# Kernel optimization log

Hardware: AMD Instinct MI355X
Metric: run time of the kernel (lower is better)

Reference implementation:

```python
import jax, jax.numpy as jnp
import numpy as np

W = 4096          # n_wavelengths
S = 4096          # n_spatial_modes
N_KEYS = 1024     # number of stored memories
SHARPNESS = 10.0  # config.retrieval_sharpness


def setup_inputs() -> dict:
    key = jax.random.key(0)
    k = jax.random.split(key, 6)
    return {
        "holo_re": jax.random.normal(k[0], (W, S), dtype=jnp.float32),
        "holo_im": jax.random.normal(k[1], (W, S), dtype=jnp.float32),
        "cue_re": jax.random.normal(k[2], (W, S), dtype=jnp.float32),
        "cue_im": jax.random.normal(k[3], (W, S), dtype=jnp.float32),
        "keys_re": jax.random.normal(k[4], (N_KEYS, W), dtype=jnp.float32),
        "keys_im": jax.random.normal(k[5], (N_KEYS, W), dtype=jnp.float32),
    }


def reference(holo_re, holo_im, cue_re, cue_im, keys_re, keys_im):
    hologram = holo_re + 1j * holo_im      # [W, S] complex64
    cue = cue_re + 1j * cue_im             # [W, S]
    keys = keys_re + 1j * keys_im          # [N, W]
    # noisy_mix = (hologram * cue.conj()).sum(dim=1)
    noisy_mix = jnp.sum(hologram * jnp.conj(cue), axis=1)  # [W]
    # torch.dot does NOT conjugate: plain complex dot per key -> batched matvec
    correlations = jnp.abs(keys @ noisy_mix)               # [N]
    attention = jax.nn.softmax(correlations * SHARPNESS)   # [N] real
    clean_key = attention.astype(keys.dtype) @ keys        # [W] complex
    out = hologram * clean_key[:, None]                    # [W, S] complex
    # return real/imag stacked so the harness compares real arrays
    return jnp.stack([out.real, out.imag])                 # [2, W, S] float32
```

## Files before the change

### kernel.cpp

```cpp
#include <hip/hip_runtime.h>
#include <math.h>

#define WDIM 4096
#define SDIM 4096
#define NKEYS 1024
#define SHARP 10.0f

__device__ __forceinline__ float wave_reduce_sum(float v) {
#pragma unroll
    for (int off = 32; off > 0; off >>= 1) v += __shfl_down(v, off, 64);
    return v;
}

__global__ __launch_bounds__(256) void k_mix(
    const float* __restrict__ hr, const float* __restrict__ hi,
    const float* __restrict__ cr, const float* __restrict__ ci,
    float* __restrict__ mix_re, float* __restrict__ mix_im) {
    const int w = blockIdx.x;
    const size_t base = (size_t)w * SDIM;
    const float4* hr4 = (const float4*)(hr + base);
    const float4* hi4 = (const float4*)(hi + base);
    const float4* cr4 = (const float4*)(cr + base);
    const float4* ci4 = (const float4*)(ci + base);
    float sr = 0.f, si = 0.f;
#pragma unroll
    for (int i = threadIdx.x; i < SDIM / 4; i += 256) {
        float4 a = hr4[i], b = hi4[i], c = cr4[i], d = ci4[i];
        sr += a.x * c.x + b.x * d.x;  si += b.x * c.x - a.x * d.x;
        sr += a.y * c.y + b.y * d.y;  si += b.y * c.y - a.y * d.y;
        sr += a.z * c.z + b.z * d.z;  si += b.z * c.z - a.z * d.z;
        sr += a.w * c.w + b.w * d.w;  si += b.w * c.w - a.w * d.w;
    }
    sr = wave_reduce_sum(sr);
    si = wave_reduce_sum(si);
    __shared__ float lre[4], lim[4];
    const int wave = threadIdx.x >> 6, lane = threadIdx.x & 63;
    if (lane == 0) { lre[wave] = sr; lim[wave] = si; }
    __syncthreads();
    if (threadIdx.x == 0) {
        mix_re[w] = lre[0] + lre[1] + lre[2] + lre[3];
        mix_im[w] = lim[0] + lim[1] + lim[2] + lim[3];
    }
}

__global__ __launch_bounds__(256) void k_corr(
    const float* __restrict__ kr, const float* __restrict__ ki,
    const float* __restrict__ mr, const float* __restrict__ mi,
    float* __restrict__ corr) {
    const int n = blockIdx.x;
    const size_t base = (size_t)n * WDIM;
    const float4* kr4 = (const float4*)(kr + base);
    const float4* ki4 = (const float4*)(ki + base);
    const float4* mr4 = (const float4*)mr;
    const float4* mi4 = (const float4*)mi;
    float zr = 0.f, zi = 0.f;
#pragma unroll
    for (int i = threadIdx.x; i < WDIM / 4; i += 256) {
        float4 a = kr4[i], b = ki4[i], m = mr4[i], q = mi4[i];
        zr += a.x * m.x - b.x * q.x;  zi += a.x * q.x + b.x * m.x;
        zr += a.y * m.y - b.y * q.y;  zi += a.y * q.y + b.y * m.y;
        zr += a.z * m.z - b.z * q.z;  zi += a.z * q.z + b.z * m.z;
        zr += a.w * m.w - b.w * q.w;  zi += a.w * q.w + b.w * m.w;
    }
    zr = wave_reduce_sum(zr);
    zi = wave_reduce_sum(zi);
    __shared__ float lre[4], lim[4];
    const int wave = threadIdx.x >> 6, lane = threadIdx.x & 63;
    if (lane == 0) { lre[wave] = zr; lim[wave] = zi; }
    __syncthreads();
    if (threadIdx.x == 0) {
        const float fr = lre[0] + lre[1] + lre[2] + lre[3];
        const float fi = lim[0] + lim[1] + lim[2] + lim[3];
        corr[n] = sqrtf(fr * fr + fi * fi) * SHARP;
    }
}

__global__ __launch_bounds__(256) void k_softmax(
    const float* __restrict__ corr, float* __restrict__ att) {
    const int t = threadIdx.x;
    __shared__ float red[256];
    float v[4];
    float m = -1e30f;
#pragma unroll
    for (int j = 0; j < 4; ++j) { v[j] = corr[t + j * 256]; m = fmaxf(m, v[j]); }
    red[t] = m; __syncthreads();
    for (int s = 128; s > 0; s >>= 1) {
        if (t < s) red[t] = fmaxf(red[t], red[t + s]);
        __syncthreads();
    }
    const float mx = red[0];
    __syncthreads();
    float e[4]; float sum = 0.f;
#pragma unroll
    for (int j = 0; j < 4; ++j) { e[j] = expf(v[j] - mx); sum += e[j]; }
    red[t] = sum; __syncthreads();
    for (int s = 128; s > 0; s >>= 1) {
        if (t < s) red[t] += red[t + s];
        __syncthreads();
    }
    const float inv = 1.0f / red[0];
#pragma unroll
    for (int j = 0; j < 4; ++j) att[t + j * 256] = e[j] * inv;
}

__global__ __launch_bounds__(256) void k_clean(
    const float* __restrict__ kr, const float* __restrict__ ki,
    const float* __restrict__ att,
    float* __restrict__ clean_re, float* __restrict__ clean_im) {
    __shared__ float s_att[NKEYS];
    for (int i = threadIdx.x; i < NKEYS; i += 256) s_att[i] = att[i];
    __syncthreads();
    const int lane = threadIdx.x & 63;
    const int grp = threadIdx.x >> 6;
    const int w = blockIdx.x * 64 + lane;
    float accr = 0.f, acci = 0.f;
    const int n0 = grp * 256;
#pragma unroll 8
    for (int n = n0; n < n0 + 256; ++n) {
        const float a = s_att[n];
        accr += a * kr[(size_t)n * WDIM + w];
        acci += a * ki[(size_t)n * WDIM + w];
    }
    __shared__ float sre[4][64], simg[4][64];
    sre[grp][lane] = accr; simg[grp][lane] = acci;
    __syncthreads();
    if (grp == 0) {
        clean_re[w] = sre[0][lane] + sre[1][lane] + sre[2][lane] + sre[3][lane];
        clean_im[w] = simg[0][lane] + simg[1][lane] + simg[2][lane] + simg[3][lane];
    }
}

__global__ __launch_bounds__(256) void k_out(
    const float* __restrict__ hr, const float* __restrict__ hi,
    const float* __restrict__ cre, const float* __restrict__ cim,
    float* __restrict__ out_re, float* __restrict__ out_im) {
    const int w = blockIdx.y;
    const size_t base = (size_t)w * SDIM;
    const int i = blockIdx.x * 256 + threadIdx.x;
    const float a = cre[w], b = cim[w];
    const float4 h = ((const float4*)(hr + base))[i];
    const float4 g = ((const float4*)(hi + base))[i];
    float4 orr, oii;
    orr.x = h.x * a - g.x * b;  oii.x = h.x * b + g.x * a;
    orr.y = h.y * a - g.y * b;  oii.y = h.y * b + g.y * a;
    orr.z = h.z * a - g.z * b;  oii.z = h.z * b + g.z * a;
    orr.w = h.w * a - g.w * b;  oii.w = h.w * b + g.w * a;
    ((float4*)(out_re + base))[i] = orr;
    ((float4*)(out_im + base))[i] = oii;
}

extern "C" void kernel_launch(void* const* d_in, const int* in_sizes, int n_in,
                              void* d_out, int out_size, void* d_ws, size_t ws_size,
                              hipStream_t stream) {
    const float* hr = (const float*)d_in[0];
    const float* hi = (const float*)d_in[1];
    const float* cr = (const float*)d_in[2];
    const float* ci = (const float*)d_in[3];
    const float* kr = (const float*)d_in[4];
    const float* ki = (const float*)d_in[5];

    float* ws = (float*)d_ws;
    float* mix_re = ws;
    float* mix_im = ws + 4096;
    float* corr   = ws + 8192;
    float* att    = ws + 9216;
    float* cre    = ws + 10240;
    float* cim    = ws + 14336;

    float* out_re = (float*)d_out;
    float* out_im = out_re + (size_t)WDIM * SDIM;

    k_mix<<<WDIM, 256, 0, stream>>>(hr, hi, cr, ci, mix_re, mix_im);
    k_corr<<<NKEYS, 256, 0, stream>>>(kr, ki, mix_re, mix_im, corr);
    k_softmax<<<1, 256, 0, stream>>>(corr, att);
    k_clean<<<WDIM / 64, 256, 0, stream>>>(kr, ki, att, cre, cim);
    k_out<<<dim3(SDIM / 1024, WDIM), 256, 0, stream>>>(hr, hi, cre, cim, out_re, out_im);
}
```

Baseline: 390.4 us.

## Rework per-wave reductions, split-N atomic clean-key, and row-per-block output kernel

k_mix and k_corr now give each wavefront its own row, which removes the shared-memory cross-wave reduction and the block barrier. k_clean is reorganised into a 2D grid that splits the key dimension into chunks of 16 and reads keys as float4. Partial sums are combined with atomicAdd into a buffer that is zeroed beforehand with a memset, which raises parallelism for the weighted key sum. k_out now processes a full row per block with four float4 iterations per thread instead of one, cutting the block count. The atomics make the clean-key summation order nondeterministic, and the extra memset adds one more operation to the stream.

After: 389.2 us. No clear change (-0.3%).

```diff
diff --git a/kernel.cpp b/kernel.cpp
--- a/kernel.cpp
+++ b/kernel.cpp
@@ -16,16 +16,18 @@
     const float* __restrict__ hr, const float* __restrict__ hi,
     const float* __restrict__ cr, const float* __restrict__ ci,
     float* __restrict__ mix_re, float* __restrict__ mix_im) {
-    const int w = blockIdx.x;
+    const int wave = threadIdx.x >> 6, lane = threadIdx.x & 63;
+    const int w = blockIdx.x * 4 + wave;
     const size_t base = (size_t)w * SDIM;
     const float4* hr4 = (const float4*)(hr + base);
     const float4* hi4 = (const float4*)(hi + base);
     const float4* cr4 = (const float4*)(cr + base);
     const float4* ci4 = (const float4*)(ci + base);
     float sr = 0.f, si = 0.f;
-#pragma unroll
-    for (int i = threadIdx.x; i < SDIM / 4; i += 256) {
-        float4 a = hr4[i], b = hi4[i], c = cr4[i], d = ci4[i];
+#pragma unroll 4
+    for (int i = 0; i < 16; ++i) {
+        const int idx = lane + i * 64;
+        float4 a = hr4[idx], b = hi4[idx], c = cr4[idx], d = ci4[idx];
         sr += a.x * c.x + b.x * d.x;  si += b.x * c.x - a.x * d.x;
         sr += a.y * c.y + b.y * d.y;  si += b.y * c.y - a.y * d.y;
         sr += a.z * c.z + b.z * d.z;  si += b.z * c.z - a.z * d.z;
@@ -33,30 +35,25 @@
     }
     sr = wave_reduce_sum(sr);
     si = wave_reduce_sum(si);
-    __shared__ float lre[4], lim[4];
-    const int wave = threadIdx.x >> 6, lane = threadIdx.x & 63;
-    if (lane == 0) { lre[wave] = sr; lim[wave] = si; }
-    __syncthreads();
-    if (threadIdx.x == 0) {
-        mix_re[w] = lre[0] + lre[1] + lre[2] + lre[3];
-        mix_im[w] = lim[0] + lim[1] + lim[2] + lim[3];
-    }
+    if (lane == 0) { mix_re[w] = sr; mix_im[w] = si; }
 }
 
 __global__ __launch_bounds__(256) void k_corr(
     const float* __restrict__ kr, const float* __restrict__ ki,
     const float* __restrict__ mr, const float* __restrict__ mi,
     float* __restrict__ corr) {
-    const int n = blockIdx.x;
+    const int wave = threadIdx.x >> 6, lane = threadIdx.x & 63;
+    const int n = blockIdx.x * 4 + wave;
     const size_t base = (size_t)n * WDIM;
     const float4* kr4 = (const float4*)(kr + base);
     const float4* ki4 = (const float4*)(ki + base);
     const float4* mr4 = (const float4*)mr;
     const float4* mi4 = (const float4*)mi;
     float zr = 0.f, zi = 0.f;
-#pragma unroll
-    for (int i = threadIdx.x; i < WDIM / 4; i += 256) {
-        float4 a = kr4[i], b = ki4[i], m = mr4[i], q = mi4[i];
+#pragma unroll 4
+    for (int i = 0; i < 16; ++i) {
+        const int idx = lane + i * 64;
+        float4 a = kr4[idx], b = ki4[idx], m = mr4[idx], q = mi4[idx];
         zr += a.x * m.x - b.x * q.x;  zi += a.x * q.x + b.x * m.x;
         zr += a.y * m.y - b.y * q.y;  zi += a.y * q.y + b.y * m.y;
         zr += a.z * m.z - b.z * q.z;  zi += a.z * q.z + b.z * m.z;
@@ -64,15 +61,7 @@
     }
     zr = wave_reduce_sum(zr);
     zi = wave_reduce_sum(zi);
-    __shared__ float lre[4], lim[4];
-    const int wave = threadIdx.x >> 6, lane = threadIdx.x & 63;
-    if (lane == 0) { lre[wave] = zr; lim[wave] = zi; }
-    __syncthreads();
-    if (threadIdx.x == 0) {
-        const float fr = lre[0] + lre[1] + lre[2] + lre[3];
-        const float fi = lim[0] + lim[1] + lim[2] + lim[3];
-        corr[n] = sqrtf(fr * fr + fi * fi) * SHARP;
-    }
+    if (lane == 0) corr[n] = sqrtf(zr * zr + zi * zi) * SHARP;
 }
 
 __global__ __launch_bounds__(256) void k_softmax(
@@ -107,46 +96,52 @@
     const float* __restrict__ kr, const float* __restrict__ ki,
     const float* __restrict__ att,
     float* __restrict__ clean_re, float* __restrict__ clean_im) {
-    __shared__ float s_att[NKEYS];
-    for (int i = threadIdx.x; i < NKEYS; i += 256) s_att[i] = att[i];
-    __syncthreads();
-    const int lane = threadIdx.x & 63;
-    const int grp = threadIdx.x >> 6;
-    const int w = blockIdx.x * 64 + lane;
-    float accr = 0.f, acci = 0.f;
-    const int n0 = grp * 256;
-#pragma unroll 8
-    for (int n = n0; n < n0 + 256; ++n) {
-        const float a = s_att[n];
-        accr += a * kr[(size_t)n * WDIM + w];
-        acci += a * ki[(size_t)n * WDIM + w];
+    const int wt = blockIdx.x;
+    const int nc = blockIdx.y;
+    const int f4 = wt * 256 + threadIdx.x;
+    const int n0 = nc * 16;
+    float4 ar = make_float4(0.f, 0.f, 0.f, 0.f);
+    float4 ai = make_float4(0.f, 0.f, 0.f, 0.f);
+#pragma unroll 4
+    for (int j = 0; j < 16; ++j) {
+        const int n = n0 + j;
+        const float a = att[n];
+        const float4 x = ((const float4*)(kr + (size_t)n * WDIM))[f4];
+        const float4 y = ((const float4*)(ki + (size_t)n * WDIM))[f4];
+        ar.x += a * x.x; ar.y += a * x.y; ar.z += a * x.z; ar.w += a * x.w;
+        ai.x += a * y.x; ai.y += a * y.y; ai.z += a * y.z; ai.w += a * y.w;
     }
-    __shared__ float sre[4][64], simg[4][64];
-    sre[grp][lane] = accr; simg[grp][lane] = acci;
-    __syncthreads();
-    if (grp == 0) {
-        clean_re[w] = sre[0][lane] + sre[1][lane] + sre[2][lane] + sre[3][lane];
-        clean_im[w] = simg[0][lane] + simg[1][lane] + simg[2][lane] + simg[3][lane];
-    }
+    const int w = f4 * 4;
+    atomicAdd(&clean_re[w + 0], ar.x); atomicAdd(&clean_re[w + 1], ar.y);
+    atomicAdd(&clean_re[w + 2], ar.z); atomicAdd(&clean_re[w + 3], ar.w);
+    atomicAdd(&clean_im[w + 0], ai.x); atomicAdd(&clean_im[w + 1], ai.y);
+    atomicAdd(&clean_im[w + 2], ai.z); atomicAdd(&clean_im[w + 3], ai.w);
 }
 
 __global__ __launch_bounds__(256) void k_out(
     const float* __restrict__ hr, const float* __restrict__ hi,
     const float* __restrict__ cre, const float* __restrict__ cim,
     float* __restrict__ out_re, float* __restrict__ out_im) {
-    const int w = blockIdx.y;
+    const int w = blockIdx.x;
     const size_t base = (size_t)w * SDIM;
-    const int i = blockIdx.x * 256 + threadIdx.x;
     const float a = cre[w], b = cim[w];
-    const float4 h = ((const float4*)(hr + base))[i];
-    const float4 g = ((const float4*)(hi + base))[i];
-    float4 orr, oii;
-    orr.x = h.x * a - g.x * b;  oii.x = h.x * b + g.x * a;
-    orr.y = h.y * a - g.y * b;  oii.y = h.y * b + g.y * a;
-    orr.z = h.z * a - g.z * b;  oii.z = h.z * b + g.z * a;
-    orr.w = h.w * a - g.w * b;  oii.w = h.w * b + g.w * a;
-    ((float4*)(out_re + base))[i] = orr;
-    ((float4*)(out_im + base))[i] = oii;
+    const float4* hr4 = (const float4*)(hr + base);
+    const float4* hi4 = (const float4*)(hi + base);
+    float4* or4 = (float4*)(out_re + base);
+    float4* oi4 = (float4*)(out_im + base);
+#pragma unroll
+    for (int j = 0; j < 4; ++j) {
+        const int i = threadIdx.x + j * 256;
+        const float4 h = hr4[i];
+        const float4 g = hi4[i];
+        float4 orr, oii;
+        orr.x = h.x * a - g.x * b;  oii.x = h.x * b + g.x * a;
+        orr.y = h.y * a - g.y * b;  oii.y = h.y * b + g.y * a;
+        orr.z = h.z * a - g.z * b;  oii.z = h.z * b + g.z * a;
+        orr.w = h.w * a - g.w * b;  oii.w = h.w * b + g.w * a;
+        or4[i] = orr;
+        oi4[i] = oii;
+    }
 }
 
 extern "C" void kernel_launch(void* const* d_in, const int* in_sizes, int n_in,
@@ -170,9 +165,10 @@
     float* out_re = (float*)d_out;
     float* out_im = out_re + (size_t)WDIM * SDIM;
 
-    k_mix<<<WDIM, 256, 0, stream>>>(hr, hi, cr, ci, mix_re, mix_im);
-    k_corr<<<NKEYS, 256, 0, stream>>>(kr, ki, mix_re, mix_im, corr);
+    k_mix<<<WDIM / 4, 256, 0, stream>>>(hr, hi, cr, ci, mix_re, mix_im);
+    k_corr<<<NKEYS / 4, 256, 0, stream>>>(kr, ki, mix_re, mix_im, corr);
     k_softmax<<<1, 256, 0, stream>>>(corr, att);
-    k_clean<<<WDIM / 64, 256, 0, stream>>>(kr, ki, att, cre, cim);
-    k_out<<<dim3(SDIM / 1024, WDIM), 256, 0, stream>>>(hr, hi, cre, cim, out_re, out_im);
+    hipMemsetAsync(cre, 0, 2 * WDIM * sizeof(float), stream);
+    k_clean<<<dim3(4, 64), 256, 0, stream>>>(kr, ki, att, cre, cim);
+    k_out<<<WDIM, 256, 0, stream>>>(hr, hi, cre, cim, out_re, out_im);
 }
```
